# Kernel optimization log

Measured on AMD Instinct MI355X. Metric: run time of the kernel, lower is better.

Reference implementation:

```python
import jax, jax.numpy as jnp
import numpy as np

B, R, C = 32, 2000, 81
BBOX_STD = np.array([0.1, 0.1, 0.2, 0.2], dtype=np.float32)
SCORE_THRESH = 0.1
IMG_W, IMG_H = 512.0, 384.0


def _decode_boxes(boxes, deltas):
    # boxes: [B,R,4] (x1,y1,x2,y2); deltas: [B,R,C,4] -> decoded [B,R,C,4]
    x1, y1, x2, y2 = boxes[..., 0], boxes[..., 1], boxes[..., 2], boxes[..., 3]
    w = x2 - x1 + 1.0
    h = y2 - y1 + 1.0
    cx = x1 + 0.5 * w
    cy = y1 + 0.5 * h
    dx, dy, dw, dh = deltas[..., 0], deltas[..., 1], deltas[..., 2], deltas[..., 3]
    pcx = dx * w[..., None] + cx[..., None]
    pcy = dy * h[..., None] + cy[..., None]
    pw = jnp.exp(dw) * w[..., None]
    ph = jnp.exp(dh) * h[..., None]
    return jnp.stack(
        [pcx - 0.5 * pw, pcy - 0.5 * ph, pcx + 0.5 * pw - 1.0, pcy + 0.5 * ph - 1.0],
        axis=-1,
    )


def setup_inputs() -> dict:
    key = jax.random.key(0)
    k1, k2, k3 = jax.random.split(key, 3)
    # proposal boxes: random well-formed (x1<=x2, y1<=y2) boxes inside the image
    corners = jax.random.uniform(k1, (B, R, 2, 2), dtype=jnp.float32) * jnp.array(
        [IMG_W, IMG_H], dtype=jnp.float32
    )
    x1y1 = jnp.min(corners, axis=2)
    x2y2 = jnp.max(corners, axis=2)
    rois = jnp.concatenate([jnp.zeros((B, R, 1), jnp.float32), x1y1, x2y2], axis=-1)
    cls_prob = jax.nn.softmax(jax.random.normal(k2, (B, R, C), dtype=jnp.float32) * 2.0, axis=-1)
    bbox_pred = jax.random.normal(k3, (B, R, 4 * C), dtype=jnp.float32) * 0.5
    return {"rois": rois, "cls_prob": cls_prob, "bbox_pred": bbox_pred}


def reference(rois, cls_prob, bbox_pred):
    b, r = rois.shape[0], rois.shape[1]
    c = cls_prob.shape[-1]
    boxes = rois[..., 1:5]  # [B,R,4]
    # delta scaling exactly as original: view(-1,4) * [0.1,0.1,0.2,0.2]
    deltas = (bbox_pred.reshape(-1, 4) * jnp.asarray(BBOX_STD)).reshape(b, r, c, 4)
    pred_boxes = _decode_boxes(boxes, deltas)  # [B,R,C,4]
    pred_boxes = jnp.maximum(pred_boxes, 0.0)  # torch.clamp(FINAL_BBOXES, 0)

    scores = cls_prob[..., 1:]          # skip background class, [B,R,C-1]
    cboxes = pred_boxes[:, :, 1:, :]    # [B,R,C-1,4]

    valid = scores > SCORE_THRESH       # score-threshold filter (inds)
    masked = jnp.where(valid, scores, -jnp.inf)
    order = jnp.argsort(-masked, axis=1)  # per-class descending sort over proposals
    sorted_scores = jnp.take_along_axis(scores, order, axis=1)
    sorted_valid = jnp.take_along_axis(valid, order, axis=1)
    sorted_boxes = jnp.take_along_axis(cboxes, order[..., None], axis=1)

    # cls_dets = [boxes | score], invalid (sub-threshold) rows zeroed instead of dropped
    dets = jnp.concatenate([sorted_boxes, sorted_scores[..., None]], axis=-1)
    dets = dets * sorted_valid[..., None].astype(dets.dtype)  # [B,R,C-1,5]

    # eval branch: softmax over class scores, max + argmax
    distribution = jax.nn.softmax(cls_prob, axis=-1)
    max_scores = jnp.max(distribution, axis=-1)
    pred_labels = jnp.argmax(distribution, axis=-1)
    return dets, sorted_valid, distribution, max_scores, pred_labels
```

## Files before the change

kernel.cpp:

```cpp
#include <hip/hip_runtime.h>
#include <hip/hip_bf16.h>
#include <math.h>

#define BB 32
#define RR 2000
#define CC 81
#define CM1 80
#define TROWS 64
#define NTILE 32
#define NTILES_TOTAL 1024
#define CAP 28
#define SCAP (NTILE * CAP)

__global__ __launch_bounds__(256) void fused1_kernel(
    const float* __restrict__ cls,
    float* __restrict__ dist,
    float* __restrict__ maxs,
    float* __restrict__ labels,
    float4* __restrict__ zbase,
    int* __restrict__ counts,
    float2* __restrict__ pairs)
{
    __shared__ float tile[CC * (TROWS + 1)];
    const int tid  = threadIdx.x;
    const int wave = tid >> 6;
    const int lane = tid & 63;

    if (blockIdx.x < NTILES_TOTAL) {
        const int b   = blockIdx.x >> 5;
        const int tr  = blockIdx.x & 31;
        const int r0  = tr * TROWS;
        const int nr  = (RR - r0 < TROWS) ? (RR - r0) : TROWS;

        const float* src = cls + (size_t)(b * RR + r0) * CC;
        for (int i = tid; i < nr * CC; i += 256) {
            int rl = i / CC, c = i - rl * CC;
            tile[c * (TROWS + 1) + rl] = src[i];
        }
        __syncthreads();

        #pragma unroll 4
        for (int q = 0; q < 20; ++q) {
            const int c   = 1 + wave + 4 * q;
            const int col = b * CM1 + (c - 1);
            float s = tile[c * (TROWS + 1) + lane];
            bool valid = (lane < nr) && (s > 0.1f);
            unsigned long long mask = __ballot(valid);
            if (valid) {
                int pos = __popcll(mask & ((1ull << lane) - 1ull));
                if (pos < CAP)
                    pairs[(size_t)col * SCAP + tr * CAP + pos] =
                        make_float2(s, __int_as_float(r0 + lane));
            }
            if (lane == 0) {
                int cnt = (int)__popcll(mask);
                counts[col * NTILE + tr] = (cnt < CAP) ? cnt : CAP;
            }
        }
        return;
    }

    const int pb = blockIdx.x - NTILES_TOTAL;

    const float4 z4 = make_float4(0.0f, 0.0f, 0.0f, 0.0f);
    const int zb = pb * 480;
    zbase[zb + tid] = z4;
    if (tid < 224) zbase[zb + 256 + tid] = z4;

    const int row = pb * 4 + wave;

    const float* in = cls + (size_t)row * CC;
    float v0 = in[lane];
    float v1 = (lane < CC - 64) ? in[64 + lane] : -INFINITY;

    float m  = v0;
    int   mi = lane;
    if (v1 > m) { m = v1; mi = 64 + lane; }

    for (int off = 32; off > 0; off >>= 1) {
        float om  = __shfl_xor(m, off);
        int   omi = __shfl_xor(mi, off);
        if (om > m || (om == m && omi < mi)) { m = om; mi = omi; }
    }

    float e0 = expf(v0 - m);
    float e1 = (lane < CC - 64) ? expf(v1 - m) : 0.0f;
    float s  = e0 + e1;
    for (int off = 32; off > 0; off >>= 1) s += __shfl_xor(s, off);

    float inv = 1.0f / s;
    float* out = dist + (size_t)row * CC;
    out[lane] = e0 * inv;
    if (lane < CC - 64) out[64 + lane] = e1 * inv;
    if (lane == 0) {
        maxs[row]   = inv;
        labels[row] = (float)mi;
    }
}

__global__ __launch_bounds__(128) void sort_decode_kernel(
    const float* __restrict__ rois,
    const float* __restrict__ bbox,
    const int* __restrict__ counts,
    const float2* __restrict__ pairs,
    float* __restrict__ dets,
    float* __restrict__ sv)
{
    __shared__ float ssc[1024];
    __shared__ int   sidx[1024];
    __shared__ int   scnt[NTILE];
    __shared__ int   spref[NTILE + 1];

    const int bj  = blockIdx.x;
    const int b   = bj / CM1;
    const int j   = bj % CM1;
    const int tid = threadIdx.x;
    const int wave = tid >> 6;
    const int lane = tid & 63;
    const int cls_col = j + 1;

    if (wave == 0) {
        int c = (lane < NTILE) ? counts[bj * NTILE + lane] : 0;
        int x = c;
        #pragma unroll
        for (int off = 1; off < NTILE; off <<= 1) {
            int v = __shfl_up(x, off);
            if (lane >= off) x += v;
        }
        if (lane < NTILE) {
            scnt[lane]  = c;
            spref[lane] = x - c;
            if (lane == NTILE - 1) spref[NTILE] = x;
        }
    }
    __syncthreads();

    const int n = spref[NTILE];
    if (n == 0) return;

    const float2* pbase = pairs + (size_t)bj * SCAP;
    for (int t = wave; t < NTILE; t += 2) {
        int cnt = scnt[t];
        for (int k = lane; k < cnt; k += 64) {
            float2 e = pbase[t * CAP + k];
            int pos = spref[t] + k;
            ssc[pos]  = e.x;
            sidx[pos] = __float_as_int(e.y);
        }
    }
    __syncthreads();

    if (n > 1) {
        if (n <= 64) {
            if (wave == 0) {
                float s  = (lane < n) ? ssc[lane]  : -INFINITY;
                int   id = (lane < n) ? sidx[lane] : 0x7FFFFFFF;
                #pragma unroll
                for (int k = 2; k <= 64; k <<= 1) {
                    #pragma unroll
                    for (int jj = k >> 1; jj > 0; jj >>= 1) {
                        float os = __shfl_xor(s, jj);
                        int   oi = __shfl_xor(id, jj);
                        bool mineFirst = (s > os) || (s == os && id < oi);
                        bool iLower = ((lane & jj) == 0);
                        bool up = ((lane & k) == 0);
                        bool keep = up ? (mineFirst == iLower)
                                       : (mineFirst != iLower);
                        if (!keep) { s = os; id = oi; }
                    }
                }
                if (lane < n) { ssc[lane] = s; sidx[lane] = id; }
            }
            __syncthreads();
        } else {
            int n2 = 1;
            while (n2 < n) n2 <<= 1;
            for (int i = n + tid; i < n2; i += 128) {
                ssc[i]  = -INFINITY;
                sidx[i] = 0x7FFFFFFF;
            }
            __syncthreads();
            for (int k = 2; k <= n2; k <<= 1) {
                for (int jj = k >> 1; jj > 0; jj >>= 1) {
                    for (int i = tid; i < n2; i += 128) {
                        int ixj = i ^ jj;
                        if (ixj > i) {
                            float si = ssc[i], sx = ssc[ixj];
                            int   ii = sidx[i], ix = sidx[ixj];
                            bool before = (si > sx) || (si == sx && ii < ix);
                            bool doswap = ((i & k) == 0) ? !before : before;
                            if (doswap) {
                                ssc[i] = sx; ssc[ixj] = si;
                                sidx[i] = ix; sidx[ixj] = ii;
                            }
                        }
                    }
                    __syncthreads();
                }
            }
        }
    }

    for (int i = tid; i < n; i += 128) {
        size_t obase = ((size_t)(b * RR + i) * CM1 + j) * 5;
        int   r = sidx[i];
        float s = ssc[i];
        const float* rp = rois + (size_t)(b * RR + r) * 5;
        float x1 = rp[1], y1 = rp[2], x2 = rp[3], y2 = rp[4];
        float w  = x2 - x1 + 1.0f;
        float h  = y2 - y1 + 1.0f;
        float cx = x1 + 0.5f * w;
        float cy = y1 + 0.5f * h;
        const float* dp = bbox + (size_t)(b * RR + r) * (4 * CC) + 4 * cls_col;
        float dx = dp[0] * 0.1f, dy = dp[1] * 0.1f;
        float dw = dp[2] * 0.2f, dh = dp[3] * 0.2f;
        float pcx = dx * w + cx;
        float pcy = dy * h + cy;
        float pw  = expf(dw) * w;
        float ph  = expf(dh) * h;
        dets[obase + 0] = fmaxf(pcx - 0.5f * pw, 0.0f);
        dets[obase + 1] = fmaxf(pcy - 0.5f * ph, 0.0f);
        dets[obase + 2] = fmaxf(pcx + 0.5f * pw - 1.0f, 0.0f);
        dets[obase + 3] = fmaxf(pcy + 0.5f * ph - 1.0f, 0.0f);
        dets[obase + 4] = s;
        sv[(size_t)(b * RR + i) * CM1 + j] = 1.0f;
    }
}

extern "C" void kernel_launch(void* const* d_in, const int* in_sizes, int n_in,
                              void* d_out, int out_size, void* d_ws, size_t ws_size,
                              hipStream_t stream) {
    const float* rois = (const float*)d_in[0];
    const float* cls  = (const float*)d_in[1];
    const float* bbox = (const float*)d_in[2];

    float* out = (float*)d_out;
    const size_t sv_off   = (size_t)BB * RR * CM1 * 5;
    const size_t dist_off = sv_off + (size_t)BB * RR * CM1;
    const size_t maxs_off = dist_off + (size_t)BB * RR * CC;
    const size_t lab_off  = maxs_off + (size_t)BB * RR;

    float* dets   = out;
    float* sv     = out + sv_off;
    float* dist   = out + dist_off;
    float* maxs   = out + maxs_off;
    float* labels = out + lab_off;

    int*    counts = (int*)d_ws;
    float2* pairs  = (float2*)((char*)d_ws + (size_t)BB * CM1 * NTILE * sizeof(int));

    fused1_kernel<<<NTILES_TOTAL + (BB * RR) / 4, 256, 0, stream>>>(
        cls, dist, maxs, labels, (float4*)dets, counts, pairs);

    sort_decode_kernel<<<BB * CM1, 128, 0, stream>>>(
        rois, bbox, counts, pairs, dets, sv);
}
```

Measured before the change: 47.68 us.

## Decode boxes in the compaction pass and gather them after the sort

Moves box decoding out of the sort kernel and into the first kernel's threshold-compaction pass. Each surviving candidate's decoded box is written to a per-column workspace buffer, and the tile position is packed into the index field. After sorting, the second kernel only gathers the precomputed float4 instead of doing scattered rois/bbox reads and exp. This takes the dependent gathers off the tail of the sort kernel, at the cost of extra workspace traffic and more work in the first kernel. The new path only runs when the workspace is large enough; otherwise the old path is used.

```diff
diff --git a/kernel.cpp b/kernel.cpp
--- a/kernel.cpp
+++ b/kernel.cpp
@@ -11,15 +11,20 @@
 #define NTILES_TOTAL 1024
 #define CAP 28
 #define SCAP (NTILE * CAP)
+#define NCOLS 2560
 
 __global__ __launch_bounds__(256) void fused1_kernel(
     const float* __restrict__ cls,
+    const float* __restrict__ rois,
+    const float* __restrict__ bbox,
     float* __restrict__ dist,
     float* __restrict__ maxs,
     float* __restrict__ labels,
     float4* __restrict__ zbase,
     int* __restrict__ counts,
-    float2* __restrict__ pairs)
+    float2* __restrict__ pairs,
+    float4* __restrict__ boxes,
+    int use_boxes)
 {
     __shared__ float tile[CC * (TROWS + 1)];
     const int tid  = threadIdx.x;
@@ -48,9 +53,36 @@
             unsigned long long mask = __ballot(valid);
             if (valid) {
                 int pos = __popcll(mask & ((1ull << lane) - 1ull));
-                if (pos < CAP)
-                    pairs[(size_t)col * SCAP + tr * CAP + pos] =
-                        make_float2(s, __int_as_float(r0 + lane));
+                if (pos < CAP) {
+                    const int tilepos = tr * CAP + pos;
+                    const int rg = r0 + lane;
+                    if (use_boxes) {
+                        const float* rp = rois + (size_t)(b * RR + rg) * 5;
+                        float x1 = rp[1], y1 = rp[2], x2 = rp[3], y2 = rp[4];
+                        float w  = x2 - x1 + 1.0f;
+                        float h  = y2 - y1 + 1.0f;
+                        float cx = x1 + 0.5f * w;
+                        float cy = y1 + 0.5f * h;
+                        const float4 d4 = *(const float4*)(bbox +
+                            (size_t)(b * RR + rg) * (4 * CC) + 4 * c);
+                        float dx = d4.x * 0.1f, dy = d4.y * 0.1f;
+                        float dw = d4.z * 0.2f, dh = d4.w * 0.2f;
+                        float pcx = dx * w + cx;
+                        float pcy = dy * h + cy;
+                        float pw  = expf(dw) * w;
+                        float ph  = expf(dh) * h;
+                        boxes[(size_t)col * SCAP + tilepos] = make_float4(
+                            fmaxf(pcx - 0.5f * pw, 0.0f),
+                            fmaxf(pcy - 0.5f * ph, 0.0f),
+                            fmaxf(pcx + 0.5f * pw - 1.0f, 0.0f),
+                            fmaxf(pcy + 0.5f * ph - 1.0f, 0.0f));
+                        pairs[(size_t)col * SCAP + tilepos] =
+                            make_float2(s, __int_as_float(rg * 1024 + tilepos));
+                    } else {
+                        pairs[(size_t)col * SCAP + tilepos] =
+                            make_float2(s, __int_as_float(rg));
+                    }
+                }
             }
             if (lane == 0) {
                 int cnt = (int)__popcll(mask);
@@ -103,8 +135,10 @@
     const float* __restrict__ bbox,
     const int* __restrict__ counts,
     const float2* __restrict__ pairs,
+    const float4* __restrict__ boxes,
     float* __restrict__ dets,
-    float* __restrict__ sv)
+    float* __restrict__ sv,
+    int use_boxes)
 {
     __shared__ float ssc[1024];
     __shared__ int   sidx[1024];
@@ -117,7 +151,6 @@
     const int tid = threadIdx.x;
     const int wave = tid >> 6;
     const int lane = tid & 63;
-    const int cls_col = j + 1;
 
     if (wave == 0) {
         int c = (lane < NTILE) ? counts[bj * NTILE + lane] : 0;
@@ -203,25 +236,34 @@
 
     for (int i = tid; i < n; i += 128) {
         size_t obase = ((size_t)(b * RR + i) * CM1 + j) * 5;
-        int   r = sidx[i];
         float s = ssc[i];
-        const float* rp = rois + (size_t)(b * RR + r) * 5;
-        float x1 = rp[1], y1 = rp[2], x2 = rp[3], y2 = rp[4];
-        float w  = x2 - x1 + 1.0f;
-        float h  = y2 - y1 + 1.0f;
-        float cx = x1 + 0.5f * w;
-        float cy = y1 + 0.5f * h;
-        const float* dp = bbox + (size_t)(b * RR + r) * (4 * CC) + 4 * cls_col;
-        float dx = dp[0] * 0.1f, dy = dp[1] * 0.1f;
-        float dw = dp[2] * 0.2f, dh = dp[3] * 0.2f;
-        float pcx = dx * w + cx;
-        float pcy = dy * h + cy;
-        float pw  = expf(dw) * w;
-        float ph  = expf(dh) * h;
-        dets[obase + 0] = fmaxf(pcx - 0.5f * pw, 0.0f);
-        dets[obase + 1] = fmaxf(pcy - 0.5f * ph, 0.0f);
-        dets[obase + 2] = fmaxf(pcx + 0.5f * pw - 1.0f, 0.0f);
-        dets[obase + 3] = fmaxf(pcy + 0.5f * ph - 1.0f, 0.0f);
+        if (use_boxes) {
+            int tilepos = sidx[i] & 1023;
+            float4 bx = boxes[(size_t)bj * SCAP + tilepos];
+            dets[obase + 0] = bx.x;
+            dets[obase + 1] = bx.y;
+            dets[obase + 2] = bx.z;
+            dets[obase + 3] = bx.w;
+        } else {
+            int   r = sidx[i];
+            const float* rp = rois + (size_t)(b * RR + r) * 5;
+            float x1 = rp[1], y1 = rp[2], x2 = rp[3], y2 = rp[4];
+            float w  = x2 - x1 + 1.0f;
+            float h  = y2 - y1 + 1.0f;
+            float cx = x1 + 0.5f * w;
+            float cy = y1 + 0.5f * h;
+            const float* dp = bbox + (size_t)(b * RR + r) * (4 * CC) + 4 * (j + 1);
+            float dx = dp[0] * 0.1f, dy = dp[1] * 0.1f;
+            float dw = dp[2] * 0.2f, dh = dp[3] * 0.2f;
+            float pcx = dx * w + cx;
+            float pcy = dy * h + cy;
+            float pw  = expf(dw) * w;
+            float ph  = expf(dh) * h;
+            dets[obase + 0] = fmaxf(pcx - 0.5f * pw, 0.0f);
+            dets[obase + 1] = fmaxf(pcy - 0.5f * ph, 0.0f);
+            dets[obase + 2] = fmaxf(pcx + 0.5f * pw - 1.0f, 0.0f);
+            dets[obase + 3] = fmaxf(pcy + 0.5f * ph - 1.0f, 0.0f);
+        }
         dets[obase + 4] = s;
         sv[(size_t)(b * RR + i) * CM1 + j] = 1.0f;
     }
@@ -246,12 +288,18 @@
     float* maxs   = out + maxs_off;
     float* labels = out + lab_off;
 
+    const size_t counts_bytes = (size_t)NCOLS * NTILE * sizeof(int);
+    const size_t pairs_bytes  = (size_t)NCOLS * SCAP * sizeof(float2);
+    const size_t boxes_bytes  = (size_t)NCOLS * SCAP * sizeof(float4);
     int*    counts = (int*)d_ws;
-    float2* pairs  = (float2*)((char*)d_ws + (size_t)BB * CM1 * NTILE * sizeof(int));
+    float2* pairs  = (float2*)((char*)d_ws + counts_bytes);
+    float4* boxes  = (float4*)((char*)d_ws + counts_bytes + pairs_bytes);
+    int use_boxes = (ws_size >= counts_bytes + pairs_bytes + boxes_bytes) ? 1 : 0;
 
     fused1_kernel<<<NTILES_TOTAL + (BB * RR) / 4, 256, 0, stream>>>(
-        cls, dist, maxs, labels, (float4*)dets, counts, pairs);
-
-    sort_decode_kernel<<<BB * CM1, 128, 0, stream>>>(
-        rois, bbox, counts, pairs, dets, sv);
+        cls, rois, bbox, dist, maxs, labels, (float4*)dets,
+        counts, pairs, boxes, use_boxes);
+
+    sort_decode_kernel<<<NCOLS, 128, 0, stream>>>(
+        rois, bbox, counts, pairs, boxes, dets, sv, use_boxes);
 }
```

Result: slower. 53.34 us (+11.9%).

## Move softmax blocks into sort kernel and widen sort blocks to 256 threads

Applied to the files above, without the earlier changes.

The per-row softmax/max/argmax work moves out of the first kernel, which now only does threshold compaction and output zeroing. It is appended as extra blocks to the sort/decode kernel, where it can fill the GPU while the per-column sort blocks, many of them small or empty, run. The sort blocks also grow from 128 to 256 threads. The cost is that the class probabilities are read again in the second kernel, and the larger sort blocks may leave threads idle when the number of candidates is small.

```diff
diff --git a/kernel.cpp b/kernel.cpp
--- a/kernel.cpp
+++ b/kernel.cpp
@@ -11,15 +11,13 @@
 #define NTILES_TOTAL 1024
 #define CAP 28
 #define SCAP (NTILE * CAP)
-
-__global__ __launch_bounds__(256) void fused1_kernel(
+#define NCOLS 2560
+
+__global__ __launch_bounds__(256) void compact_zero_kernel(
     const float* __restrict__ cls,
-    float* __restrict__ dist,
-    float* __restrict__ maxs,
-    float* __restrict__ labels,
-    float4* __restrict__ zbase,
     int* __restrict__ counts,
-    float2* __restrict__ pairs)
+    float2* __restrict__ pairs,
+    float4* __restrict__ zbase)
 {
     __shared__ float tile[CC * (TROWS + 1)];
     const int tid  = threadIdx.x;
@@ -60,170 +58,177 @@
         return;
     }
 
-    const int pb = blockIdx.x - NTILES_TOTAL;
-
+    const int zb = (blockIdx.x - NTILES_TOTAL) * 480;
     const float4 z4 = make_float4(0.0f, 0.0f, 0.0f, 0.0f);
-    const int zb = pb * 480;
     zbase[zb + tid] = z4;
     if (tid < 224) zbase[zb + 256 + tid] = z4;
-
-    const int row = pb * 4 + wave;
-
-    const float* in = cls + (size_t)row * CC;
-    float v0 = in[lane];
-    float v1 = (lane < CC - 64) ? in[64 + lane] : -INFINITY;
-
-    float m  = v0;
-    int   mi = lane;
-    if (v1 > m) { m = v1; mi = 64 + lane; }
-
-    for (int off = 32; off > 0; off >>= 1) {
-        float om  = __shfl_xor(m, off);
-        int   omi = __shfl_xor(mi, off);
-        if (om > m || (om == m && omi < mi)) { m = om; mi = omi; }
-    }
-
-    float e0 = expf(v0 - m);
-    float e1 = (lane < CC - 64) ? expf(v1 - m) : 0.0f;
-    float s  = e0 + e1;
-    for (int off = 32; off > 0; off >>= 1) s += __shfl_xor(s, off);
-
-    float inv = 1.0f / s;
-    float* out = dist + (size_t)row * CC;
-    out[lane] = e0 * inv;
-    if (lane < CC - 64) out[64 + lane] = e1 * inv;
-    if (lane == 0) {
-        maxs[row]   = inv;
-        labels[row] = (float)mi;
-    }
 }
 
-__global__ __launch_bounds__(128) void sort_decode_kernel(
+__global__ __launch_bounds__(256) void sort_softmax_kernel(
     const float* __restrict__ rois,
     const float* __restrict__ bbox,
+    const float* __restrict__ cls,
     const int* __restrict__ counts,
     const float2* __restrict__ pairs,
     float* __restrict__ dets,
-    float* __restrict__ sv)
+    float* __restrict__ sv,
+    float* __restrict__ dist,
+    float* __restrict__ maxs,
+    float* __restrict__ labels)
 {
     __shared__ float ssc[1024];
     __shared__ int   sidx[1024];
     __shared__ int   scnt[NTILE];
     __shared__ int   spref[NTILE + 1];
 
-    const int bj  = blockIdx.x;
-    const int b   = bj / CM1;
-    const int j   = bj % CM1;
-    const int tid = threadIdx.x;
+    const int tid  = threadIdx.x;
     const int wave = tid >> 6;
     const int lane = tid & 63;
-    const int cls_col = j + 1;
-
-    if (wave == 0) {
-        int c = (lane < NTILE) ? counts[bj * NTILE + lane] : 0;
-        int x = c;
-        #pragma unroll
-        for (int off = 1; off < NTILE; off <<= 1) {
-            int v = __shfl_up(x, off);
-            if (lane >= off) x += v;
-        }
-        if (lane < NTILE) {
-            scnt[lane]  = c;
-            spref[lane] = x - c;
-            if (lane == NTILE - 1) spref[NTILE] = x;
-        }
-    }
-    __syncthreads();
-
-    const int n = spref[NTILE];
-    if (n == 0) return;
-
-    const float2* pbase = pairs + (size_t)bj * SCAP;
-    for (int t = wave; t < NTILE; t += 2) {
-        int cnt = scnt[t];
-        for (int k = lane; k < cnt; k += 64) {
-            float2 e = pbase[t * CAP + k];
-            int pos = spref[t] + k;
-            ssc[pos]  = e.x;
-            sidx[pos] = __float_as_int(e.y);
-        }
-    }
-    __syncthreads();
-
-    if (n > 1) {
-        if (n <= 64) {
-            if (wave == 0) {
-                float s  = (lane < n) ? ssc[lane]  : -INFINITY;
-                int   id = (lane < n) ? sidx[lane] : 0x7FFFFFFF;
-                #pragma unroll
-                for (int k = 2; k <= 64; k <<= 1) {
+
+    if (blockIdx.x < NCOLS) {
+        const int bj = blockIdx.x;
+        const int b  = bj / CM1;
+        const int j  = bj % CM1;
+        const int cls_col = j + 1;
+
+        if (wave == 0) {
+            int c = (lane < NTILE) ? counts[bj * NTILE + lane] : 0;
+            int x = c;
+            #pragma unroll
+            for (int off = 1; off < NTILE; off <<= 1) {
+                int v = __shfl_up(x, off);
+                if (lane >= off) x += v;
+            }
+            if (lane < NTILE) {
+                scnt[lane]  = c;
+                spref[lane] = x - c;
+                if (lane == NTILE - 1) spref[NTILE] = x;
+            }
+        }
+        __syncthreads();
+
+        const int n = spref[NTILE];
+        if (n == 0) return;
+
+        const float2* pbase = pairs + (size_t)bj * SCAP;
+        for (int t = wave; t < NTILE; t += 4) {
+            int cnt = scnt[t];
+            for (int k = lane; k < cnt; k += 64) {
+                float2 e = pbase[t * CAP + k];
+                int pos = spref[t] + k;
+                ssc[pos]  = e.x;
+                sidx[pos] = __float_as_int(e.y);
+            }
+        }
+        __syncthreads();
+
+        if (n > 1) {
+            if (n <= 64) {
+                if (wave == 0) {
+                    float s  = (lane < n) ? ssc[lane]  : -INFINITY;
+                    int   id = (lane < n) ? sidx[lane] : 0x7FFFFFFF;
                     #pragma unroll
+                    for (int k = 2; k <= 64; k <<= 1) {
+                        #pragma unroll
+                        for (int jj = k >> 1; jj > 0; jj >>= 1) {
+                            float os = __shfl_xor(s, jj);
+                            int   oi = __shfl_xor(id, jj);
+                            bool mineFirst = (s > os) || (s == os && id < oi);
+                            bool iLower = ((lane & jj) == 0);
+                            bool up = ((lane & k) == 0);
+                            bool keep = up ? (mineFirst == iLower)
+                                           : (mineFirst != iLower);
+                            if (!keep) { s = os; id = oi; }
+                        }
+                    }
+                    if (lane < n) { ssc[lane] = s; sidx[lane] = id; }
+                }
+                __syncthreads();
+            } else {
+                int n2 = 1;
+                while (n2 < n) n2 <<= 1;
+                for (int i = n + tid; i < n2; i += 256) {
+                    ssc[i]  = -INFINITY;
+                    sidx[i] = 0x7FFFFFFF;
+                }
+                __syncthreads();
+                for (int k = 2; k <= n2; k <<= 1) {
                     for (int jj = k >> 1; jj > 0; jj >>= 1) {
-                        float os = __shfl_xor(s, jj);
-                        int   oi = __shfl_xor(id, jj);
-                        bool mineFirst = (s > os) || (s == os && id < oi);
-                        bool iLower = ((lane & jj) == 0);
-                        bool up = ((lane & k) == 0);
-                        bool keep = up ? (mineFirst == iLower)
-                                       : (mineFirst != iLower);
-                        if (!keep) { s = os; id = oi; }
+                        for (int i = tid; i < n2; i += 256) {
+                            int ixj = i ^ jj;
+                            if (ixj > i) {
+                                float si = ssc[i], sx = ssc[ixj];
+                                int   ii = sidx[i], ix = sidx[ixj];
+                                bool before = (si > sx) || (si == sx && ii < ix);
+                                bool doswap = ((i & k) == 0) ? !before : before;
+                                if (doswap) {
+                                    ssc[i] = sx; ssc[ixj] = si;
+                                    sidx[i] = ix; sidx[ixj] = ii;
+                                }
+                            }
+                        }
+                        __syncthreads();
                     }
                 }
-                if (lane < n) { ssc[lane] = s; sidx[lane] = id; }
-            }
-            __syncthreads();
-        } else {
-            int n2 = 1;
-            while (n2 < n) n2 <<= 1;
-            for (int i = n + tid; i < n2; i += 128) {
-                ssc[i]  = -INFINITY;
-                sidx[i] = 0x7FFFFFFF;
-            }
-            __syncthreads();
-            for (int k = 2; k <= n2; k <<= 1) {
-                for (int jj = k >> 1; jj > 0; jj >>= 1) {
-                    for (int i = tid; i < n2; i += 128) {
-                        int ixj = i ^ jj;
-                        if (ixj > i) {
-                            float si = ssc[i], sx = ssc[ixj];
-                            int   ii = sidx[i], ix = sidx[ixj];
-                            bool before = (si > sx) || (si == sx && ii < ix);
-                            bool doswap = ((i & k) == 0) ? !before : before;
-                            if (doswap) {
-                                ssc[i] = sx; ssc[ixj] = si;
-                                sidx[i] = ix; sidx[ixj] = ii;
-                            }
-                        }
-                    }
-                    __syncthreads();
-                }
-            }
-        }
-    }
-
-    for (int i = tid; i < n; i += 128) {
-        size_t obase = ((size_t)(b * RR + i) * CM1 + j) * 5;
-        int   r = sidx[i];
-        float s = ssc[i];
-        const float* rp = rois + (size_t)(b * RR + r) * 5;
-        float x1 = rp[1], y1 = rp[2], x2 = rp[3], y2 = rp[4];
-        float w  = x2 - x1 + 1.0f;
-        float h  = y2 - y1 + 1.0f;
-        float cx = x1 + 0.5f * w;
-        float cy = y1 + 0.5f * h;
-        const float* dp = bbox + (size_t)(b * RR + r) * (4 * CC) + 4 * cls_col;
-        float dx = dp[0] * 0.1f, dy = dp[1] * 0.1f;
-        float dw = dp[2] * 0.2f, dh = dp[3] * 0.2f;
-        float pcx = dx * w + cx;
-        float pcy = dy * h + cy;
-        float pw  = expf(dw) * w;
-        float ph  = expf(dh) * h;
-        dets[obase + 0] = fmaxf(pcx - 0.5f * pw, 0.0f);
-        dets[obase + 1] = fmaxf(pcy - 0.5f * ph, 0.0f);
-        dets[obase + 2] = fmaxf(pcx + 0.5f * pw - 1.0f, 0.0f);
-        dets[obase + 3] = fmaxf(pcy + 0.5f * ph - 1.0f, 0.0f);
-        dets[obase + 4] = s;
-        sv[(size_t)(b * RR + i) * CM1 + j] = 1.0f;
+            }
+        }
+
+        for (int i = tid; i < n; i += 256) {
+            size_t obase = ((size_t)(b * RR + i) * CM1 + j) * 5;
+            int   r = sidx[i];
+            float s = ssc[i];
+            const float* rp = rois + (size_t)(b * RR + r) * 5;
+            float x1 = rp[1], y1 = rp[2], x2 = rp[3], y2 = rp[4];
+            float w  = x2 - x1 + 1.0f;
+            float h  = y2 - y1 + 1.0f;
+            float cx = x1 + 0.5f * w;
+            float cy = y1 + 0.5f * h;
+            const float* dp = bbox + (size_t)(b * RR + r) * (4 * CC) + 4 * cls_col;
+            float dx = dp[0] * 0.1f, dy = dp[1] * 0.1f;
+            float dw = dp[2] * 0.2f, dh = dp[3] * 0.2f;
+            float pcx = dx * w + cx;
+            float pcy = dy * h + cy;
+            float pw  = expf(dw) * w;
+            float ph  = expf(dh) * h;
+            dets[obase + 0] = fmaxf(pcx - 0.5f * pw, 0.0f);
+            dets[obase + 1] = fmaxf(pcy - 0.5f * ph, 0.0f);
+            dets[obase + 2] = fmaxf(pcx + 0.5f * pw - 1.0f, 0.0f);
+            dets[obase + 3] = fmaxf(pcy + 0.5f * ph - 1.0f, 0.0f);
+            dets[obase + 4] = s;
+            sv[(size_t)(b * RR + i) * CM1 + j] = 1.0f;
+        }
+        return;
+    }
+
+    const int pb  = blockIdx.x - NCOLS;
+    const int row = pb * 4 + wave;
+
+    const float* in = cls + (size_t)row * CC;
+    float v0 = in[lane];
+    float v1 = (lane < CC - 64) ? in[64 + lane] : -INFINITY;
+
+    float m  = v0;
+    int   mi = lane;
+    if (v1 > m) { m = v1; mi = 64 + lane; }
+
+    for (int off = 32; off > 0; off >>= 1) {
+        float om  = __shfl_xor(m, off);
+        int   omi = __shfl_xor(mi, off);
+        if (om > m || (om == m && omi < mi)) { m = om; mi = omi; }
+    }
+
+    float e0 = expf(v0 - m);
+    float e1 = (lane < CC - 64) ? expf(v1 - m) : 0.0f;
+    float s  = e0 + e1;
+    for (int off = 32; off > 0; off >>= 1) s += __shfl_xor(s, off);
+
+    float inv = 1.0f / s;
+    float* outd = dist + (size_t)row * CC;
+    outd[lane] = e0 * inv;
+    if (lane < CC - 64) outd[64 + lane] = e1 * inv;
+    if (lane == 0) {
+        maxs[row]   = inv;
+        labels[row] = (float)mi;
     }
 }
 
@@ -247,11 +252,11 @@
     float* labels = out + lab_off;
 
     int*    counts = (int*)d_ws;
-    float2* pairs  = (float2*)((char*)d_ws + (size_t)BB * CM1 * NTILE * sizeof(int));
-
-    fused1_kernel<<<NTILES_TOTAL + (BB * RR) / 4, 256, 0, stream>>>(
-        cls, dist, maxs, labels, (float4*)dets, counts, pairs);
-
-    sort_decode_kernel<<<BB * CM1, 128, 0, stream>>>(
-        rois, bbox, counts, pairs, dets, sv);
+    float2* pairs  = (float2*)((char*)d_ws + (size_t)NCOLS * NTILE * sizeof(int));
+
+    compact_zero_kernel<<<NTILES_TOTAL + (BB * RR) / 4, 256, 0, stream>>>(
+        cls, counts, pairs, (float4*)dets);
+
+    sort_softmax_kernel<<<NCOLS + (BB * RR) / 4, 256, 0, stream>>>(
+        rois, bbox, cls, counts, pairs, dets, sv, dist, maxs, labels);
 }
```

Result: slower. 51.33 us (+7.7%).

## Prefetch roi/bbox rows into cache and sort up to 128 entries in registers

Applied to the files above, without the earlier changes.

The first kernel now issues dummy loads of the rois and the per-class bbox deltas for valid entries, with an empty asm keeping them alive. This warms the L2/MALL cache for the decode step in the second kernel. The sort kernel gives up the LDS staging for n<=128: each lane binary-searches the tile prefix sums to fetch its own pair and runs a two-wave register bitonic sort with one LDS merge step. Decode follows without extra barriers. The prefetch adds memory traffic to the first kernel, and its value depends on those lines staying cached.

```diff
diff --git a/kernel.cpp b/kernel.cpp
--- a/kernel.cpp
+++ b/kernel.cpp
@@ -11,9 +11,12 @@
 #define NTILES_TOTAL 1024
 #define CAP 28
 #define SCAP (NTILE * CAP)
+#define NCOLS 2560
 
 __global__ __launch_bounds__(256) void fused1_kernel(
     const float* __restrict__ cls,
+    const float* __restrict__ rois,
+    const float* __restrict__ bbox,
     float* __restrict__ dist,
     float* __restrict__ maxs,
     float* __restrict__ labels,
@@ -36,6 +39,12 @@
         for (int i = tid; i < nr * CC; i += 256) {
             int rl = i / CC, c = i - rl * CC;
             tile[c * (TROWS + 1) + rl] = src[i];
+        }
+
+        if (wave == 0 && lane < nr) {
+            const float4 rv = *(const float4*)(rois +
+                (size_t)(b * RR + r0 + lane) * 5 + 1);
+            asm volatile("" :: "v"(rv.x), "v"(rv.y), "v"(rv.z), "v"(rv.w));
         }
         __syncthreads();
 
@@ -51,6 +60,9 @@
                 if (pos < CAP)
                     pairs[(size_t)col * SCAP + tr * CAP + pos] =
                         make_float2(s, __int_as_float(r0 + lane));
+                const float4 d4 = *(const float4*)(bbox +
+                    (size_t)(b * RR + r0 + lane) * (4 * CC) + 4 * c);
+                asm volatile("" :: "v"(d4.x), "v"(d4.y), "v"(d4.z), "v"(d4.w));
             }
             if (lane == 0) {
                 int cnt = (int)__popcll(mask);
@@ -119,85 +131,143 @@
     const int lane = tid & 63;
     const int cls_col = j + 1;
 
-    if (wave == 0) {
-        int c = (lane < NTILE) ? counts[bj * NTILE + lane] : 0;
-        int x = c;
+    int c = (lane < NTILE) ? counts[bj * NTILE + lane] : 0;
+    int x = c;
+    #pragma unroll
+    for (int off = 1; off < NTILE; off <<= 1) {
+        int v = __shfl_up(x, off);
+        if (lane >= off) x += v;
+    }
+    const int e = x - c;
+    const int n = __shfl(x, NTILE - 1);
+    if (n == 0) return;
+
+    const float2* pbase = pairs + (size_t)bj * SCAP;
+
+    if (n <= 128) {
+        const int g = (wave << 6) | lane;
+
+        int lo = 0;
         #pragma unroll
-        for (int off = 1; off < NTILE; off <<= 1) {
-            int v = __shfl_up(x, off);
-            if (lane >= off) x += v;
-        }
-        if (lane < NTILE) {
-            scnt[lane]  = c;
-            spref[lane] = x - c;
-            if (lane == NTILE - 1) spref[NTILE] = x;
-        }
+        for (int st = 16; st > 0; st >>= 1) {
+            int p = lo + st;
+            int v = __shfl(e, (p < NTILE) ? p : 0);
+            if (p < NTILE && v <= g) lo = p;
+        }
+        int base = __shfl(e, lo);
+
+        float s; int id;
+        if (g < n) {
+            float2 pr = pbase[lo * CAP + (g - base)];
+            s  = pr.x;
+            id = __float_as_int(pr.y);
+        } else {
+            s  = -INFINITY;
+            id = 0x7FFFFFFF;
+        }
+
+        const bool asc = (wave == 1);
+        #pragma unroll
+        for (int k = 2; k <= 64; k <<= 1) {
+            #pragma unroll
+            for (int jj = k >> 1; jj > 0; jj >>= 1) {
+                float os = __shfl_xor(s, jj);
+                int   oi = __shfl_xor(id, jj);
+                bool mineFirst = (s > os) || (s == os && id < oi);
+                if (asc) mineFirst = !mineFirst;
+                bool iLower = ((lane & jj) == 0);
+                bool up = ((lane & k) == 0);
+                bool keep = up ? (mineFirst == iLower) : (mineFirst != iLower);
+                if (!keep) { s = os; id = oi; }
+            }
+        }
+
+        ssc[tid]  = s;
+        sidx[tid] = id;
+        __syncthreads();
+        {
+            float os = ssc[tid ^ 64];
+            int   oi = sidx[tid ^ 64];
+            bool mineFirst = (s > os) || (s == os && id < oi);
+            bool iLower = (wave == 0);
+            if (mineFirst != iLower) { s = os; id = oi; }
+        }
+        #pragma unroll
+        for (int jj = 32; jj > 0; jj >>= 1) {
+            float os = __shfl_xor(s, jj);
+            int   oi = __shfl_xor(id, jj);
+            bool mineFirst = (s > os) || (s == os && id < oi);
+            bool iLower = ((lane & jj) == 0);
+            if (mineFirst != iLower) { s = os; id = oi; }
+        }
+
+        if (g < n) {
+            size_t obase = ((size_t)(b * RR + g) * CM1 + j) * 5;
+            int   r = id;
+            const float* rp = rois + (size_t)(b * RR + r) * 5;
+            float x1 = rp[1], y1 = rp[2], x2 = rp[3], y2 = rp[4];
+            float w  = x2 - x1 + 1.0f;
+            float h  = y2 - y1 + 1.0f;
+            float cx = x1 + 0.5f * w;
+            float cy = y1 + 0.5f * h;
+            const float* dp = bbox + (size_t)(b * RR + r) * (4 * CC) + 4 * cls_col;
+            float dx = dp[0] * 0.1f, dy = dp[1] * 0.1f;
+            float dw = dp[2] * 0.2f, dh = dp[3] * 0.2f;
+            float pcx = dx * w + cx;
+            float pcy = dy * h + cy;
+            float pw  = expf(dw) * w;
+            float ph  = expf(dh) * h;
+            dets[obase + 0] = fmaxf(pcx - 0.5f * pw, 0.0f);
+            dets[obase + 1] = fmaxf(pcy - 0.5f * ph, 0.0f);
+            dets[obase + 2] = fmaxf(pcx + 0.5f * pw - 1.0f, 0.0f);
+            dets[obase + 3] = fmaxf(pcy + 0.5f * ph - 1.0f, 0.0f);
+            dets[obase + 4] = s;
+            sv[(size_t)(b * RR + g) * CM1 + j] = 1.0f;
+        }
+        return;
+    }
+
+    if (wave == 0 && lane < NTILE) {
+        scnt[lane]  = c;
+        spref[lane] = e;
+        if (lane == NTILE - 1) spref[NTILE] = n;
     }
     __syncthreads();
 
-    const int n = spref[NTILE];
-    if (n == 0) return;
-
-    const float2* pbase = pairs + (size_t)bj * SCAP;
     for (int t = wave; t < NTILE; t += 2) {
         int cnt = scnt[t];
         for (int k = lane; k < cnt; k += 64) {
-            float2 e = pbase[t * CAP + k];
+            float2 pe = pbase[t * CAP + k];
             int pos = spref[t] + k;
-            ssc[pos]  = e.x;
-            sidx[pos] = __float_as_int(e.y);
+            ssc[pos]  = pe.x;
+            sidx[pos] = __float_as_int(pe.y);
         }
     }
     __syncthreads();
 
-    if (n > 1) {
-        if (n <= 64) {
-            if (wave == 0) {
-                float s  = (lane < n) ? ssc[lane]  : -INFINITY;
-                int   id = (lane < n) ? sidx[lane] : 0x7FFFFFFF;
-                #pragma unroll
-                for (int k = 2; k <= 64; k <<= 1) {
-                    #pragma unroll
-                    for (int jj = k >> 1; jj > 0; jj >>= 1) {
-                        float os = __shfl_xor(s, jj);
-                        int   oi = __shfl_xor(id, jj);
-                        bool mineFirst = (s > os) || (s == os && id < oi);
-                        bool iLower = ((lane & jj) == 0);
-                        bool up = ((lane & k) == 0);
-                        bool keep = up ? (mineFirst == iLower)
-                                       : (mineFirst != iLower);
-                        if (!keep) { s = os; id = oi; }
+    int n2 = 1;
+    while (n2 < n) n2 <<= 1;
+    for (int i = n + tid; i < n2; i += 128) {
+        ssc[i]  = -INFINITY;
+        sidx[i] = 0x7FFFFFFF;
+    }
+    __syncthreads();
+    for (int k = 2; k <= n2; k <<= 1) {
+        for (int jj = k >> 1; jj > 0; jj >>= 1) {
+            for (int i = tid; i < n2; i += 128) {
+                int ixj = i ^ jj;
+                if (ixj > i) {
+                    float si = ssc[i], sx = ssc[ixj];
+                    int   ii = sidx[i], ix = sidx[ixj];
+                    bool before = (si > sx) || (si == sx && ii < ix);
+                    bool doswap = ((i & k) == 0) ? !before : before;
+                    if (doswap) {
+                        ssc[i] = sx; ssc[ixj] = si;
+                        sidx[i] = ix; sidx[ixj] = ii;
                     }
                 }
-                if (lane < n) { ssc[lane] = s; sidx[lane] = id; }
             }
             __syncthreads();
-        } else {
-            int n2 = 1;
-            while (n2 < n) n2 <<= 1;
-            for (int i = n + tid; i < n2; i += 128) {
-                ssc[i]  = -INFINITY;
-                sidx[i] = 0x7FFFFFFF;
-            }
-            __syncthreads();
-            for (int k = 2; k <= n2; k <<= 1) {
-                for (int jj = k >> 1; jj > 0; jj >>= 1) {
-                    for (int i = tid; i < n2; i += 128) {
-                        int ixj = i ^ jj;
-                        if (ixj > i) {
-                            float si = ssc[i], sx = ssc[ixj];
-                            int   ii = sidx[i], ix = sidx[ixj];
-                            bool before = (si > sx) || (si == sx && ii < ix);
-                            bool doswap = ((i & k) == 0) ? !before : before;
-                            if (doswap) {
-                                ssc[i] = sx; ssc[ixj] = si;
-                                sidx[i] = ix; sidx[ixj] = ii;
-                            }
-                        }
-                    }
-                    __syncthreads();
-                }
-            }
         }
     }
 
@@ -247,11 +317,11 @@
     float* labels = out + lab_off;
 
     int*    counts = (int*)d_ws;
-    float2* pairs  = (float2*)((char*)d_ws + (size_t)BB * CM1 * NTILE * sizeof(int));
+    float2* pairs  = (float2*)((char*)d_ws + (size_t)NCOLS * NTILE * sizeof(int));
 
     fused1_kernel<<<NTILES_TOTAL + (BB * RR) / 4, 256, 0, stream>>>(
-        cls, dist, maxs, labels, (float4*)dets, counts, pairs);
-
-    sort_decode_kernel<<<BB * CM1, 128, 0, stream>>>(
+        cls, rois, bbox, dist, maxs, labels, (float4*)dets, counts, pairs);
+
+    sort_decode_kernel<<<NCOLS, 128, 0, stream>>>(
         rois, bbox, counts, pairs, dets, sv);
 }
```

Measured after the change: 45.28 us. 5.0% less time.
